# Kernel optimization log

Measured on AMD Instinct MI355X. Metric: run time of the kernel, lower is better.

Reference implementation:

```python
import jax, jax.numpy as jnp
import numpy as np

WS, OWS, NHEAD = 4, 6, 6          # window, overlap window = 4 + int(0.5*4), heads
B, CIN, COU, H, W = 2, 192, 192, 224, 224
MID = CIN  # r = 1


def calc_rpi_oca(ws=WS, ows=OWS):
    # relative position index between ws x ws query window and ows x ows overlapping kv window
    co = np.stack(np.meshgrid(np.arange(ws), np.arange(ws), indexing='ij')).reshape(2, -1)
    ce = np.stack(np.meshgrid(np.arange(ows), np.arange(ows), indexing='ij')).reshape(2, -1)
    rel = (ce[:, None, :] - co[:, :, None]).transpose(1, 2, 0) + (ws - 1)  # [ws*ws, ows*ows, 2], >= 0
    idx = rel[..., 0] * (ws + ows - 1) + rel[..., 1]                       # in [0, (ws+ows-1)^2)
    return jnp.asarray(idx)  # [16, 36]

RPI = calc_rpi_oca()


def conv2d(x, w, b, pad):
    out = jax.lax.conv_general_dilated(x, w, (1, 1), [(pad, pad), (pad, pad)],
                                       dimension_numbers=('NCHW', 'OIHW', 'NCHW'))
    return out + b[None, :, None, None]


def group_norm(x, g, b, groups, eps=1e-5):
    n = x.shape[0]
    xg = x.reshape(n, groups, -1)
    mu = xg.mean(-1, keepdims=True)
    var = xg.var(-1, keepdims=True)
    xn = ((xg - mu) * jax.lax.rsqrt(var + eps)).reshape(x.shape)
    return xn * g[None, :, None, None] + b[None, :, None, None]


def layer_norm(x, g, b, eps=1e-5):
    mu = x.mean(-1, keepdims=True)
    var = x.var(-1, keepdims=True)
    return (x - mu) * jax.lax.rsqrt(var + eps) * g + b


def ocab(x, h, w, ln1_g, ln1_b, qkv_w, qkv_b, rpb, proj_w, proj_b,
         ln2_g, ln2_b, fc1_w, fc1_b, fc2_w, fc2_b):
    b, _, c = x.shape
    nh, nw, d = h // WS, w // WS, c // NHEAD
    shortcut = x
    xn = layer_norm(x, ln1_g, ln1_b).reshape(b, h, w, c)
    qkv = xn @ qkv_w + qkv_b                                  # [b,h,w,3c] laid out [q|k|v]
    q = qkv[..., :c]
    kv = jnp.stack([qkv[..., c:2 * c], qkv[..., 2 * c:]])     # [2,b,h,w,c]
    # non-overlapping query windows -> [b*nwin, 16, NHEAD, d]
    qw = q.reshape(b, nh, WS, nw, WS, c).transpose(0, 1, 3, 2, 4, 5).reshape(b * nh * nw, WS * WS, NHEAD, d)
    # overlapping kv windows = Unfold(kernel=OWS, stride=WS, pad=(OWS-WS)//2)
    pad = (OWS - WS) // 2
    kvp = jnp.pad(kv, ((0, 0), (0, 0), (pad, pad), (pad, pad), (0, 0)))
    rows = (jnp.arange(nh) * WS)[:, None] + jnp.arange(OWS)[None, :]   # [nh, OWS]
    cols = (jnp.arange(nw) * WS)[:, None] + jnp.arange(OWS)[None, :]   # [nw, OWS]
    patches = kvp[:, :, rows[:, None, :, None], cols[None, :, None, :], :]  # [2,b,nh,nw,OWS,OWS,c]
    kvw = patches.reshape(2, b * nh * nw, OWS * OWS, NHEAD, d)
    kw, vw = kvw[0], kvw[1]
    attn = jnp.einsum('wqhd,wkhd->whqk', qw * (d ** -0.5), kw)  # [b*nwin, NHEAD, 16, 36]
    bias = rpb[RPI.reshape(-1)].reshape(WS * WS, OWS * OWS, NHEAD).transpose(2, 0, 1)
    attn = jax.nn.softmax(attn + bias[None], axis=-1)
    out = jnp.einsum('whqk,wkhd->wqhd', attn, vw).reshape(b, nh, nw, WS, WS, c)
    out = out.transpose(0, 1, 3, 2, 4, 5).reshape(b, h * w, c)  # window_reverse
    out = out @ proj_w + proj_b + shortcut
    xm = layer_norm(out, ln2_g, ln2_b)
    mlp = jax.nn.gelu(xm @ fc1_w + fc1_b, approximate=False) @ fc2_w + fc2_b
    return out + mlp


def atoca_forward(x, conv1_w, conv1_b, gn1_g, gn1_b, conv2_w, conv2_b, gn2_g, gn2_b,
                  conv3_w, conv3_b, ln1_g, ln1_b, qkv_w, qkv_b, rpb, proj_w, proj_b,
                  ln2_g, ln2_b, fc1_w, fc1_b, fc2_w, fc2_b):
    Bx, C, Hx, Wx = x.shape
    shortcut = x
    # raw row-major reshape, exactly as the torch code (not a spatial window partition)
    out = x.reshape(Bx * (Hx // WS) * (Wx // WS), C, WS, WS)
    out = conv2d(out, conv1_w, conv1_b, 1)
    out = jax.nn.silu(group_norm(out, gn1_g, gn1_b, NHEAD))
    out = out.transpose(0, 2, 3, 1).reshape(Bx, Hx * Wx, -1)
    out = ocab(out, Hx, Wx, ln1_g, ln1_b, qkv_w, qkv_b, rpb, proj_w, proj_b,
               ln2_g, ln2_b, fc1_w, fc1_b, fc2_w, fc2_b)
    out = out.reshape(Bx * (Hx // WS) * (Wx // WS), WS, WS, -1).transpose(0, 3, 1, 2)
    out = conv2d(out, conv2_w, conv2_b, 1)
    out = group_norm(out, gn2_g, gn2_b, NHEAD)
    out = out.reshape(Bx, -1, Hx, Wx)
    out = out + conv2d(shortcut, conv3_w, conv3_b, 0)
    return jax.nn.relu(out)


def setup_inputs() -> dict:
    key = jax.random.key(0)
    ks = iter(jax.random.split(key, 32))
    rn = lambda shape, s=0.02: (s * jax.random.normal(next(ks), shape)).astype(jnp.float32)
    return {
        'x': jax.random.normal(next(ks), (B, CIN, H, W), dtype=jnp.float32),
        'conv1_w': rn((MID, CIN, 3, 3)), 'conv1_b': rn((MID,)),
        'gn1_g': jnp.ones((MID,), jnp.float32), 'gn1_b': jnp.zeros((MID,), jnp.float32),
        'conv2_w': rn((COU, MID, 3, 3)), 'conv2_b': rn((COU,)),
        'gn2_g': jnp.ones((COU,), jnp.float32), 'gn2_b': jnp.zeros((COU,), jnp.float32),
        'conv3_w': rn((COU, CIN, 1, 1)), 'conv3_b': rn((COU,)),
        'ln1_g': jnp.ones((MID,), jnp.float32), 'ln1_b': jnp.zeros((MID,), jnp.float32),
        'qkv_w': rn((MID, 3 * MID)), 'qkv_b': rn((3 * MID,)),
        'rpb': rn(((WS + OWS - 1) ** 2, NHEAD)),
        'proj_w': rn((MID, MID)), 'proj_b': rn((MID,)),
        'ln2_g': jnp.ones((MID,), jnp.float32), 'ln2_b': jnp.zeros((MID,), jnp.float32),
        'fc1_w': rn((MID, 2 * MID)), 'fc1_b': rn((2 * MID,)),
        'fc2_w': rn((2 * MID, MID)), 'fc2_b': rn((MID,)),
    }


def reference(x, conv1_w, conv1_b, gn1_g, gn1_b, conv2_w, conv2_b, gn2_g, gn2_b,
              conv3_w, conv3_b, ln1_g, ln1_b, qkv_w, qkv_b, rpb, proj_w, proj_b,
              ln2_g, ln2_b, fc1_w, fc1_b, fc2_w, fc2_b):
    return atoca_forward(x, conv1_w, conv1_b, gn1_g, gn1_b, conv2_w, conv2_b, gn2_g, gn2_b,
                         conv3_w, conv3_b, ln1_g, ln1_b, qkv_w, qkv_b, rpb, proj_w, proj_b,
                         ln2_g, ln2_b, fc1_w, fc1_b, fc2_w, fc2_b)
```

## Files before the change

kernel.cpp:

```cpp
#include <hip/hip_runtime.h>
#include <hip/hip_bf16.h>
#include <math.h>

typedef __hip_bfloat16 bf16;
typedef __attribute__((ext_vector_type(8))) short s8v;
typedef __attribute__((ext_vector_type(4))) short s4v;
typedef __attribute__((ext_vector_type(4))) float f32x4;
typedef __attribute__((ext_vector_type(2))) _Float16 h2;

constexpr int CB   = 2;
constexpr int CH   = 224, CW = 224;
constexpr int NHW  = 56;
constexpr int NPATCH = CB * NHW * NHW;
constexpr int TOKPB  = CH * CW;
constexpr int MTOK   = CB * TOKPB;
constexpr size_t SECSZ = 19267584;

constexpr size_t B_T0  = 0;
constexpr size_t B_P2  = B_T0 + 38535168;
constexpr size_t B_P3  = B_P2 + 115605504;
constexpr size_t B_P4  = B_P3 + 38535168;
constexpr size_t B_WF1 = B_P4 + 38535168;
constexpr size_t B_WF2 = B_WF1 + 1327104;
constexpr size_t B_W3F = B_WF2 + 1327104;
constexpr size_t B_WQ  = B_W3F + 147456;
constexpr size_t B_WP  = B_WQ + 221184;
constexpr size_t B_WG1 = B_WP + 73728;
constexpr size_t B_WG2 = B_WG1 + 147456;
constexpr size_t WS_NEEDED = B_WG2 + 147456;

__device__ __forceinline__ float ldf(const float* p) { return *p; }
__device__ __forceinline__ float ldf(const bf16* p)  { return __bfloat162float(*p); }
__device__ __forceinline__ void  stf(float* p, float v) { *p = v; }
__device__ __forceinline__ void  stf(bf16* p, float v)  { *p = __float2bfloat16(v); }
__device__ __forceinline__ unsigned short f2bf(float f) {
    unsigned u = __builtin_bit_cast(unsigned, f);
    unsigned r = (u + 0x7fffu + ((u >> 16) & 1u)) >> 16;
    return (unsigned short)r;
}
__device__ __forceinline__ float bf2f(short s) {
    unsigned u = ((unsigned)(unsigned short)s) << 16;
    return __builtin_bit_cast(float, u);
}

__device__ __forceinline__ void prep_wf(const float* __restrict__ w, short* __restrict__ wf, int o) {
    int within = o & 511, frag = o >> 9;
    int l = within >> 3, j = within & 7;
    int nt = frag % 12, t2 = frag / 12, ks = t2 % 6, tap = t2 / 6;
    int co = nt * 16 + (l & 15);
    int ci = ks * 32 + (l >> 4) * 8 + j;
    wf[o] = (short)f2bf(w[(co * 192 + ci) * 9 + tap]);
}
__device__ __forceinline__ void prep_wgemm(const float* __restrict__ w, short* __restrict__ wf,
                                           int K, int N, int o) {
    int j = o & 7, l = (o >> 3) & 63, f = o >> 9;
    int ntiles = N >> 4;
    int kt = f / ntiles, nt = f % ntiles;
    int k = kt * 32 + (l >> 4) * 8 + j;
    int col = nt * 16 + (l & 15);
    wf[o] = (short)f2bf(w[(size_t)k * N + col]);
}
__device__ __forceinline__ void prep_w3f(const float* __restrict__ w, short* __restrict__ wf, int o) {
    int j = o & 7, l = (o >> 3) & 63, f = o >> 9;
    int kt = f / 12, ct = f % 12;
    int co = ct * 16 + (l & 15);
    int ci = kt * 32 + (l >> 4) * 8 + j;
    wf[o] = (short)f2bf(w[co * 192 + ci]);
}
__global__ __launch_bounds__(256) void prep_all_kernel(
    const float* __restrict__ conv1_w, short* __restrict__ WF1,
    const float* __restrict__ conv2_w, short* __restrict__ WF2,
    const float* __restrict__ conv3_w, short* __restrict__ W3F,
    const float* __restrict__ qkv_w,   short* __restrict__ WQ,
    const float* __restrict__ proj_w,  short* __restrict__ WP,
    const float* __restrict__ fc1_w,   short* __restrict__ WG1,
    const float* __restrict__ fc2_w,   short* __restrict__ WG2)
{
    int o = blockIdx.x * 256 + threadIdx.x;
    if (o < 331776)            { prep_wf(conv1_w, WF1, o); return; }
    o -= 331776;
    if (o < 331776)            { prep_wf(conv2_w, WF2, o); return; }
    o -= 331776;
    if (o < 36864)             { prep_w3f(conv3_w, W3F, o); return; }
    o -= 36864;
    if (o < 110592)            { prep_wgemm(qkv_w, WQ, 192, 576, o); return; }
    o -= 110592;
    if (o < 36864)             { prep_wgemm(proj_w, WP, 192, 192, o); return; }
    o -= 36864;
    if (o < 73728)             { prep_wgemm(fc1_w, WG1, 192, 384, o); return; }
    o -= 73728;
    if (o < 73728)             { prep_wgemm(fc2_w, WG2, 384, 192, o); return; }
}
constexpr int PREP_TOTAL = 331776 * 2 + 36864 + 110592 + 36864 + 73728 * 2;

template <bool FIRST>
__global__ __launch_bounds__(256, 4) void conv_mfma_kernel(
    const void* __restrict__ srcv, const short* __restrict__ wf,
    const float* __restrict__ bias, const float* __restrict__ gng,
    const float* __restrict__ gnb, bf16* __restrict__ dst)
{
    __shared__ short xs[13056];
    __shared__ float gsum[4][6], gsum2[4][6], gmu[4][6], grs[4][6];
    const int tid  = threadIdx.x;
    const int lane = tid & 63, wid = tid >> 6;
    const int n0   = blockIdx.x * 4;

    if (tid < 24) { gsum[tid / 6][tid % 6] = 0.f; gsum2[tid / 6][tid % 6] = 0.f; }
    for (int u = tid; u < 4 * 192; u += 256) {
        int q = u / 192;
        xs[q * 3264 + 3072 + (u % 192)] = 0;
    }

    if constexpr (FIRST) {
        const float4* sp = (const float4*)((const float*)srcv + (size_t)n0 * 3072);
        #pragma unroll
        for (int u = 0; u < 12; ++u) {
            int idx = u * 256 + tid;
            float4 v = sp[idx];
            int q = idx / 768;
            int li = (idx % 768) * 4;
            int ci = li >> 4, p0 = li & 15;
            float vv[4] = { v.x, v.y, v.z, v.w };
            #pragma unroll
            for (int k = 0; k < 4; ++k) {
                int row = p0 + k;
                int ba = q * 6528 + ((row * 384 + ci * 2) ^ ((row & 7) << 4));
                *(short*)((char*)xs + ba) = (short)f2bf(vv[k]);
            }
        }
    } else {
        const s8v* sp8 = (const s8v*)((const bf16*)srcv + (size_t)n0 * 3072);
        #pragma unroll
        for (int u = 0; u < 6; ++u) {
            int li = u * 256 + tid;
            int r = li / 24, ch = li % 24;
            int q = r >> 4, rl = r & 15;
            s8v val = sp8[li];
            int ba = q * 6528 + ((rl * 384 + ch * 16) ^ ((rl & 7) << 4));
            *(s8v*)((char*)xs + ba) = val;
        }
    }
    __syncthreads();

    const int ntb = wid * 3;
    const int cl  = lane & 15;
    const int kg  = lane >> 4;
    f32x4 acc[3][4];
    #pragma unroll
    for (int t = 0; t < 3; ++t) {
        float bv = bias[(ntb + t) * 16 + cl];
        #pragma unroll
        for (int q = 0; q < 4; ++q) acc[t][q] = (f32x4){ bv, bv, bv, bv };
    }

    const int pi = cl >> 2, pj = cl & 3;
    const s8v* wf8 = (const s8v*)wf;

    for (int tap = 0; tap < 9; ++tap) {
        const int di = tap / 3, dj = tap % 3;
        const int ii = pi + di - 1, jj = pj + dj - 1;
        const bool valid = (ii >= 0 && ii < 4 && jj >= 0 && jj < 4);
        const int nr  = valid ? (ii * 4 + jj) : 16;
        const int rb  = nr * 384;
        const int swz = (nr & 7) << 4;
        #pragma unroll
        for (int ks = 0; ks < 6; ++ks) {
            const s8v* bp = wf8 + (size_t)((tap * 6 + ks) * 12) * 64 + lane;
            s8v b0 = bp[(ntb + 0) * 64];
            s8v b1 = bp[(ntb + 1) * 64];
            s8v b2 = bp[(ntb + 2) * 64];
            const int inner = (rb + ks * 64 + kg * 16) ^ swz;
            #pragma unroll
            for (int q = 0; q < 4; ++q) {
                s8v a = *(const s8v*)((const char*)xs + q * 6528 + inner);
                acc[0][q] = __builtin_amdgcn_mfma_f32_16x16x32_bf16(a, b0, acc[0][q], 0, 0, 0);
                acc[1][q] = __builtin_amdgcn_mfma_f32_16x16x32_bf16(a, b1, acc[1][q], 0, 0, 0);
                acc[2][q] = __builtin_amdgcn_mfma_f32_16x16x32_bf16(a, b2, acc[2][q], 0, 0, 0);
            }
        }
    }

    #pragma unroll
    for (int t = 0; t < 3; ++t) {
        const int g = (ntb + t) >> 1;
        #pragma unroll
        for (int q = 0; q < 4; ++q) {
            f32x4 A = acc[t][q];
            float s  = A[0] + A[1] + A[2] + A[3];
            float s2 = A[0]*A[0] + A[1]*A[1] + A[2]*A[2] + A[3]*A[3];
            #pragma unroll
            for (int off = 32; off; off >>= 1) { s += __shfl_xor(s, off); s2 += __shfl_xor(s2, off); }
            if (lane == 0) { atomicAdd(&gsum[q][g], s); atomicAdd(&gsum2[q][g], s2); }
        }
    }
    __syncthreads();
    if (tid < 24) {
        int q = tid / 6, g = tid % 6;
        float mu  = gsum[q][g] * (1.f / 512.f);
        float var = gsum2[q][g] * (1.f / 512.f) - mu * mu;
        gmu[q][g] = mu; grs[q][g] = rsqrtf(var + 1e-5f);
    }
    __syncthreads();

    if constexpr (FIRST) {
        #pragma unroll
        for (int t = 0; t < 3; ++t) {
            const int co = (ntb + t) * 16 + cl, g = (ntb + t) >> 1;
            const float gg = gng[co], gb = gnb[co];
            #pragma unroll
            for (int q = 0; q < 4; ++q) {
                const float mu = gmu[q][g], rs = grs[q][g];
                #pragma unroll
                for (int r = 0; r < 4; ++r) {
                    float v = (acc[t][q][r] - mu) * rs * gg + gb;
                    v = v / (1.f + __expf(-v));
                    int row = q * 16 + kg * 4 + r;
                    int ba = (row * 384 + co * 2) ^ ((row & 7) << 4);
                    *(short*)((char*)xs + ba) = (short)f2bf(v);
                }
            }
        }
        __syncthreads();
        bf16* dp = dst + (size_t)n0 * 3072;
        #pragma unroll
        for (int u = 0; u < 6; ++u) {
            int li = u * 256 + tid;
            int row = li / 24, g2 = li % 24;
            int ba = (row * 384 + g2 * 16) ^ ((row & 7) << 4);
            s8v val = *(const s8v*)((const char*)xs + ba);
            *(s8v*)(dp + (size_t)row * 192 + g2 * 8) = val;
        }
    } else {
        #pragma unroll
        for (int t = 0; t < 3; ++t) {
            const int co = (ntb + t) * 16 + cl, g = (ntb + t) >> 1;
            const float gg = gng[co], gb = gnb[co];
            #pragma unroll
            for (int q = 0; q < 4; ++q) {
                const float mu = gmu[q][g], rs = grs[q][g];
                #pragma unroll
                for (int r = 0; r < 4; ++r) {
                    float v = (acc[t][q][r] - mu) * rs * gg + gb;
                    xs[q * 3072 + co * 16 + kg * 4 + r] = (short)f2bf(v);
                }
            }
        }
        __syncthreads();
        s4v* dp = (s4v*)(dst + (size_t)n0 * 3072);
        const s4v* sps = (const s4v*)xs;
        #pragma unroll
        for (int u = 0; u < 12; ++u) {
            dp[u * 256 + tid] = sps[u * 256 + tid];
        }
    }
}

template <bool RES, bool GELU_ACT, bool LN, bool QKVOUT, int NKT>
__global__ __launch_bounds__(256) void gemm_mfma_kernel(
    const bf16* __restrict__ A, const short* __restrict__ wfb,
    const float* __restrict__ bias, const bf16* __restrict__ res,
    void* __restrict__ out, int N,
    const float* __restrict__ lng, const float* __restrict__ lnb)
{
    __shared__ short ls[8192];
    const int tid = threadIdx.x, lane = tid & 63, wid = tid >> 6;
    const int m0 = blockIdx.x * 128;
    const int cl = lane & 15, kg = lane >> 4;
    constexpr int K = NKT * 32;
    const int ntiles = N >> 4;
    const int ntsec = ntiles / gridDim.y;
    const int ntbeg = blockIdx.y * ntsec;

    s8v af0[NKT], af1[NKT];
    const int r0 = m0 + wid * 32 + cl;
    #pragma unroll
    for (int kt = 0; kt < NKT; ++kt) {
        af0[kt] = *(const s8v*)(A + (size_t)r0 * K + kt * 32 + kg * 8);
        af1[kt] = *(const s8v*)(A + (size_t)(r0 + 16) * K + kt * 32 + kg * 8);
    }
    if constexpr (LN) {
        static_assert(!LN || NKT == 6, "LN requires K==192");
        #pragma unroll
        for (int r = 0; r < 2; ++r) {
            s8v* af = r ? af1 : af0;
            float s = 0.f, s2 = 0.f;
            #pragma unroll
            for (int kt = 0; kt < NKT; ++kt)
                #pragma unroll
                for (int j = 0; j < 8; ++j) {
                    float v = bf2f(af[kt][j]);
                    s += v; s2 += v * v;
                }
            s  += __shfl_xor(s, 16);  s2 += __shfl_xor(s2, 16);
            s  += __shfl_xor(s, 32);  s2 += __shfl_xor(s2, 32);
            const float mu = s * (1.f / 192.f);
            const float rs = rsqrtf(s2 * (1.f / 192.f) - mu * mu + 1e-5f);
            #pragma unroll
            for (int kt = 0; kt < NKT; ++kt) {
                const float* gp = lng + kt * 32 + kg * 8;
                const float* bp = lnb + kt * 32 + kg * 8;
                #pragma unroll
                for (int j = 0; j < 8; ++j) {
                    float v = (bf2f(af[kt][j]) - mu) * rs * gp[j] + bp[j];
                    af[kt][j] = (short)f2bf(v);
                }
            }
        }
    }

    const s8v* wf8 = (const s8v*)wfb;
    for (int nt0 = ntbeg; nt0 < ntbeg + ntsec; nt0 += 4) {
        const int n0 = nt0 * 16;
        f32x4 acc[2][4];
        #pragma unroll
        for (int nf = 0; nf < 4; ++nf) {
            float bv = bias[n0 + nf * 16 + cl];
            acc[0][nf] = (f32x4){ bv, bv, bv, bv };
            acc[1][nf] = (f32x4){ bv, bv, bv, bv };
        }
        #pragma unroll
        for (int kt = 0; kt < NKT; ++kt) {
            #pragma unroll
            for (int nf = 0; nf < 4; ++nf) {
                s8v b = wf8[(size_t)(kt * ntiles + nt0 + nf) * 64 + lane];
                acc[0][nf] = __builtin_amdgcn_mfma_f32_16x16x32_bf16(af0[kt], b, acc[0][nf], 0, 0, 0);
                acc[1][nf] = __builtin_amdgcn_mfma_f32_16x16x32_bf16(af1[kt], b, acc[1][nf], 0, 0, 0);
            }
        }

        __syncthreads();
        #pragma unroll
        for (int rf = 0; rf < 2; ++rf) {
            #pragma unroll
            for (int nf = 0; nf < 4; ++nf) {
                const int lcol = nf * 16 + cl;
                #pragma unroll
                for (int r = 0; r < 4; ++r) {
                    const int lrow = wid * 32 + rf * 16 + kg * 4 + r;
                    float v = acc[rf][nf][r];
                    if (GELU_ACT) v = 0.5f * v * (1.f + erff(v * 0.70710678118f));
                    short sv;
                    if constexpr (QKVOUT) sv = __builtin_bit_cast(short, (_Float16)v);
                    else                  sv = (short)f2bf(v);
                    int ba = (lrow * 128 + lcol * 2) ^ ((lrow & 7) << 4);
                    *(short*)((char*)ls + ba) = sv;
                }
            }
        }
        __syncthreads();
        #pragma unroll
        for (int p = 0; p < 4; ++p) {
            const int lrow = p * 32 + (tid >> 3);
            const int g = tid & 7;
            int ba = (lrow * 128 + g * 16) ^ ((lrow & 7) << 4);
            s8v val = *(const s8v*)((const char*)ls + ba);
            const int row = m0 + lrow;
            const int col0 = n0 + g * 8;
            if constexpr (QKVOUT) {
                const int sec = n0 / 192;
                const int c0 = col0 - sec * 192, h = c0 >> 5, d0 = c0 & 31;
                const int bb2 = row / TOKPB, t = row - bb2 * TOKPB;
                *(s8v*)((_Float16*)out + (size_t)sec * SECSZ +
                        ((size_t)(bb2 * 6 + h) * TOKPB + t) * 32 + d0) = val;
            } else if constexpr (RES) {
                s8v rv = *(const s8v*)(res + (size_t)row * N + col0);
                s8v ov;
                #pragma unroll
                for (int e = 0; e < 8; ++e) ov[e] = (short)f2bf(bf2f(val[e]) + bf2f(rv[e]));
                *(s8v*)((bf16*)out + (size_t)row * N + col0) = ov;
            } else {
                *(s8v*)((bf16*)out + (size_t)row * N + col0) = val;
            }
        }
    }
}

constexpr int HSTR = 1160;
__global__ __launch_bounds__(128) void attn_kernel(
    const _Float16* __restrict__ qf, const float* __restrict__ rpb,
    bf16* __restrict__ out)
{
    __shared__ short kh[6 * HSTR];
    __shared__ short vh[6 * HSTR];
    const int w = blockIdx.x;
    const int b = w / (NHW * NHW), wi = w % (NHW * NHW);
    const int nhi = wi / NHW, nwi = wi % NHW;
    const int tid = threadIdx.x;
    const int r0 = nhi * 4 - 1, c0 = nwi * 4 - 1;
    const _Float16* kfb = qf + SECSZ;
    const _Float16* vfb = qf + 2 * SECSZ;

    #pragma unroll
    for (int it = 0; it < 14; ++it) {
        int v = tid + it * 128;
        if (v < 1728) {
            int kv = v >= 864 ? 1 : 0;
            int u = v - kv * 864;
            int h = u / 144, rem = u % 144, kj = rem >> 2, d0 = (rem & 3) * 8;
            int rr = r0 + kj / 6, cc = c0 + kj % 6;
            s8v val = { 0, 0, 0, 0, 0, 0, 0, 0 };
            if (rr >= 0 && rr < CH && cc >= 0 && cc < CW) {
                const _Float16* src = kv ? vfb : kfb;
                val = *(const s8v*)(src + ((size_t)(b * 6 + h) * TOKPB + rr * CW + cc) * 32 + d0);
            }
            short* dst = kv ? vh : kh;
            *(s8v*)(dst + h * HSTR + kj * 32 + d0) = val;
        }
    }
    __syncthreads();

    if (tid < 96) {
        const int h = tid >> 4, qi = tid & 15;
        const int qr = nhi * 4 + (qi >> 2), qc = nwi * 4 + (qi & 3);
        const _Float16* qp = qf + ((size_t)(b * 6 + h) * TOKPB + qr * CW + qc) * 32;
        h2 qh[16];
        #pragma unroll
        for (int u = 0; u < 4; ++u) {
            uint4 qa = *(const uint4*)(qp + u * 8);
            qh[u * 4 + 0] = __builtin_bit_cast(h2, qa.x);
            qh[u * 4 + 1] = __builtin_bit_cast(h2, qa.y);
            qh[u * 4 + 2] = __builtin_bit_cast(h2, qa.z);
            qh[u * 4 + 3] = __builtin_bit_cast(h2, qa.w);
        }

        float sc[36];
        const short* khb = kh + h * HSTR;
        #pragma unroll
        for (int kj = 0; kj < 36; ++kj) {
            const uint4* kp = (const uint4*)(khb + kj * 32);
            uint4 k0 = kp[0], k1 = kp[1], k2 = kp[2], k3 = kp[3];
            unsigned kwv[16] = { k0.x, k0.y, k0.z, k0.w, k1.x, k1.y, k1.z, k1.w,
                                 k2.x, k2.y, k2.z, k2.w, k3.x, k3.y, k3.z, k3.w };
            float a0 = 0.f, a1 = 0.f, a2 = 0.f, a3 = 0.f;
            #pragma unroll
            for (int e = 0; e < 4; ++e) {
                a0 = __builtin_amdgcn_fdot2(__builtin_bit_cast(h2, kwv[4*e+0]), qh[4*e+0], a0, false);
                a1 = __builtin_amdgcn_fdot2(__builtin_bit_cast(h2, kwv[4*e+1]), qh[4*e+1], a1, false);
                a2 = __builtin_amdgcn_fdot2(__builtin_bit_cast(h2, kwv[4*e+2]), qh[4*e+2], a2, false);
                a3 = __builtin_amdgcn_fdot2(__builtin_bit_cast(h2, kwv[4*e+3]), qh[4*e+3], a3, false);
            }
            const int rel0 = kj / 6 - (qi >> 2) + 3;
            const int rel1 = kj % 6 - (qi & 3) + 3;
            sc[kj] = ((a0 + a1) + (a2 + a3)) * 0.17677669529f + rpb[(rel0 * 9 + rel1) * 6 + h];
        }
        float mx = -1e30f;
        #pragma unroll
        for (int kj = 0; kj < 36; ++kj) mx = fmaxf(mx, sc[kj]);
        float sum = 0.f;
        #pragma unroll
        for (int kj = 0; kj < 36; ++kj) { sc[kj] = __expf(sc[kj] - mx); sum += sc[kj]; }
        const float inv = 1.f / sum;

        h2 o2[16];
        #pragma unroll
        for (int e = 0; e < 16; ++e) o2[e] = (h2){ (_Float16)0.f, (_Float16)0.f };
        const short* vhb = vh + h * HSTR;
        #pragma unroll
        for (int kj = 0; kj < 36; ++kj) {
            const uint4* vp = (const uint4*)(vhb + kj * 32);
            uint4 v0 = vp[0], v1 = vp[1], v2 = vp[2], v3 = vp[3];
            unsigned vwv[16] = { v0.x, v0.y, v0.z, v0.w, v1.x, v1.y, v1.z, v1.w,
                                 v2.x, v2.y, v2.z, v2.w, v3.x, v3.y, v3.z, v3.w };
            const _Float16 ph = (_Float16)sc[kj];
            const h2 ph2 = { ph, ph };
            #pragma unroll
            for (int e = 0; e < 16; ++e)
                o2[e] = __builtin_bit_cast(h2, vwv[e]) * ph2 + o2[e];
        }
        bf16* op = out + ((size_t)(b * TOKPB + qr * CW + qc)) * 192 + h * 32;
        #pragma unroll
        for (int u = 0; u < 8; ++u) {
            s4v pk;
            #pragma unroll
            for (int e = 0; e < 2; ++e) {
                h2 ov = o2[u * 2 + e];
                pk[2 * e]     = (short)f2bf((float)ov[0] * inv);
                pk[2 * e + 1] = (short)f2bf((float)ov[1] * inv);
            }
            *(s4v*)((bf16*)op + u * 4) = pk;
        }
    }
}

__global__ __launch_bounds__(256, 4) void final_mfma_kernel(
    const float* __restrict__ x, const short* __restrict__ w3f,
    const float* __restrict__ b3, const bf16* __restrict__ c2,
    float* __restrict__ out)
{
    __shared__ short xs2[12288];
    const int pix0 = blockIdx.x * 64;
    const int b    = blockIdx.y;
    const int tid = threadIdx.x, lane = tid & 63, wid = tid >> 6;
    const int cl = lane & 15, kg = lane >> 4;
    const float* xb = x + (size_t)b * (192 * TOKPB);

    #pragma unroll
    for (int u = 0; u < 12; ++u) {
        int idx = u * 256 + tid;
        int ci = idx >> 4, p4 = (idx & 15) << 2;
        float4 v = *(const float4*)(xb + (size_t)ci * TOKPB + pix0 + p4);
        float vv[4] = { v.x, v.y, v.z, v.w };
        #pragma unroll
        for (int k = 0; k < 4; ++k) {
            int row = p4 + k;
            int ba = (row * 384 + ci * 2) ^ ((row & 7) << 4);
            *(short*)((char*)xs2 + ba) = (short)f2bf(vv[k]);
        }
    }
    __syncthreads();

    const int ctb = wid * 3;
    f32x4 acc[3][4] = {};
    const s8v* wf8 = (const s8v*)w3f;

    #pragma unroll
    for (int kt = 0; kt < 6; ++kt) {
        s8v a0 = wf8[(size_t)(kt * 12 + ctb + 0) * 64 + lane];
        s8v a1 = wf8[(size_t)(kt * 12 + ctb + 1) * 64 + lane];
        s8v a2 = wf8[(size_t)(kt * 12 + ctb + 2) * 64 + lane];
        #pragma unroll
        for (int pt = 0; pt < 4; ++pt) {
            int row = pt * 16 + cl;
            int ba = (row * 384 + kt * 64 + kg * 16) ^ ((row & 7) << 4);
            s8v bfr = *(const s8v*)((const char*)xs2 + ba);
            acc[0][pt] = __builtin_amdgcn_mfma_f32_16x16x32_bf16(a0, bfr, acc[0][pt], 0, 0, 0);
            acc[1][pt] = __builtin_amdgcn_mfma_f32_16x16x32_bf16(a1, bfr, acc[1][pt], 0, 0, 0);
            acc[2][pt] = __builtin_amdgcn_mfma_f32_16x16x32_bf16(a2, bfr, acc[2][pt], 0, 0, 0);
        }
    }

    #pragma unroll
    for (int t = 0; t < 3; ++t) {
        #pragma unroll
        for (int r = 0; r < 4; ++r) {
            const int co = (ctb + t) * 16 + kg * 4 + r;
            const float bb = b3[co];
            const size_t rowbase = (size_t)b * (192 * TOKPB) + (size_t)co * TOKPB + pix0;
            #pragma unroll
            for (int pt = 0; pt < 4; ++pt) {
                const size_t f = rowbase + pt * 16 + cl;
                float v = acc[t][pt][r] + bb + bf2f(__builtin_bit_cast(short, c2[f]));
                out[f] = fmaxf(v, 0.f);
            }
        }
    }
}

extern "C" void kernel_launch(void* const* d_in, const int* in_sizes, int n_in,
                              void* d_out, int out_size, void* d_ws, size_t ws_size,
                              hipStream_t stream)
{
    if (ws_size < WS_NEEDED) return;

    const float* x       = (const float*)d_in[0];
    const float* conv1_w = (const float*)d_in[1];
    const float* conv1_b = (const float*)d_in[2];
    const float* gn1_g   = (const float*)d_in[3];
    const float* gn1_b   = (const float*)d_in[4];
    const float* conv2_w = (const float*)d_in[5];
    const float* conv2_b = (const float*)d_in[6];
    const float* gn2_g   = (const float*)d_in[7];
    const float* gn2_b   = (const float*)d_in[8];
    const float* conv3_w = (const float*)d_in[9];
    const float* conv3_b = (const float*)d_in[10];
    const float* ln1_g   = (const float*)d_in[11];
    const float* ln1_b   = (const float*)d_in[12];
    const float* qkv_w   = (const float*)d_in[13];
    const float* qkv_b   = (const float*)d_in[14];
    const float* rpb     = (const float*)d_in[15];
    const float* proj_w  = (const float*)d_in[16];
    const float* proj_b  = (const float*)d_in[17];
    const float* ln2_g   = (const float*)d_in[18];
    const float* ln2_b   = (const float*)d_in[19];
    const float* fc1_w   = (const float*)d_in[20];
    const float* fc1_b   = (const float*)d_in[21];
    const float* fc2_w   = (const float*)d_in[22];
    const float* fc2_b   = (const float*)d_in[23];

    char* wsb = (char*)d_ws;
    bf16*  T0  = (bf16*)(wsb + B_T0);
    _Float16* QF = (_Float16*)(wsb + B_P2);
    bf16*  HID = (bf16*)(wsb + B_P2);
    bf16*  P3  = (bf16*)(wsb + B_P3);
    bf16*  P4  = (bf16*)(wsb + B_P4);
    short* WF1 = (short*)(wsb + B_WF1);
    short* WF2 = (short*)(wsb + B_WF2);
    short* W3F = (short*)(wsb + B_W3F);
    short* WQ  = (short*)(wsb + B_WQ);
    short* WP  = (short*)(wsb + B_WP);
    short* WG1 = (short*)(wsb + B_WG1);
    short* WG2 = (short*)(wsb + B_WG2);
    float* OUT = (float*)d_out;

    prep_all_kernel<<<(PREP_TOTAL + 255) / 256, 256, 0, stream>>>(
        conv1_w, WF1, conv2_w, WF2, conv3_w, W3F, qkv_w, WQ, proj_w, WP, fc1_w, WG1, fc2_w, WG2);

    conv_mfma_kernel<true><<<NPATCH / 4, 256, 0, stream>>>(x, WF1, conv1_b, gn1_g, gn1_b, T0);
    gemm_mfma_kernel<false, false, true, true, 6><<<dim3(MTOK / 128, 1), 256, 0, stream>>>(
        T0, WQ, qkv_b, nullptr, QF, 576, ln1_g, ln1_b);
    attn_kernel<<<NPATCH, 128, 0, stream>>>(QF, rpb, P3);
    gemm_mfma_kernel<true, false, false, false, 6><<<dim3(MTOK / 128, 1), 256, 0, stream>>>(
        P3, WP, proj_b, T0, P4, 192, nullptr, nullptr);
    gemm_mfma_kernel<false, true, true, false, 6><<<dim3(MTOK / 128, 1), 256, 0, stream>>>(
        P4, WG1, fc1_b, nullptr, HID, 384, ln2_g, ln2_b);
    gemm_mfma_kernel<true, false, false, false, 12><<<dim3(MTOK / 128, 1), 256, 0, stream>>>(
        HID, WG2, fc2_b, P4, P3, 192, nullptr, nullptr);
    conv_mfma_kernel<false><<<NPATCH / 4, 256, 0, stream>>>(P3, WF2, conv2_b, gn2_g, gn2_b, P4);
    final_mfma_kernel<<<dim3(TOKPB / 64, CB), 256, 0, stream>>>(x, W3F, conv3_b, P4, OUT);
}
```

Baseline: 576.2 us.

## Fuse attention output projection and residual add into attention kernel

The attention kernel now stages its per-window 16x192 output in shared memory and runs the proj GEMM there with MFMA, adding the bias and the T0 residual before writing P4. This removes the separate proj GEMM launch and the round trip of the attention output through global memory. In exchange each 128-thread block reloads the full proj weight fragments from global or L2, only two waves share the MFMA work, and the extra syncthreads and LDS reuse add latency to an already small block.

```diff
diff --git a/kernel.cpp b/kernel.cpp
--- a/kernel.cpp
+++ b/kernel.cpp
@@ -376,16 +376,18 @@
 }
 
 constexpr int HSTR = 1160;
-__global__ __launch_bounds__(128) void attn_kernel(
+__global__ __launch_bounds__(128) void attn_proj_kernel(
     const _Float16* __restrict__ qf, const float* __restrict__ rpb,
-    bf16* __restrict__ out)
+    const short* __restrict__ wpf, const float* __restrict__ pb,
+    const bf16* __restrict__ t0, bf16* __restrict__ omid)
 {
-    __shared__ short kh[6 * HSTR];
-    __shared__ short vh[6 * HSTR];
+    __shared__ __align__(16) short kh[6 * HSTR];
+    __shared__ __align__(16) short vh[6 * HSTR];
     const int w = blockIdx.x;
     const int b = w / (NHW * NHW), wi = w % (NHW * NHW);
     const int nhi = wi / NHW, nwi = wi % NHW;
     const int tid = threadIdx.x;
+    const int lane = tid & 63, wid = tid >> 6;
     const int r0 = nhi * 4 - 1, c0 = nwi * 4 - 1;
     const _Float16* kfb = qf + SECSZ;
     const _Float16* vfb = qf + 2 * SECSZ;
@@ -409,6 +411,8 @@
     }
     __syncthreads();
 
+    h2 o2[16];
+    float inv = 0.f;
     if (tid < 96) {
         const int h = tid >> 4, qi = tid & 15;
         const int qr = nhi * 4 + (qi >> 2), qc = nwi * 4 + (qi & 3);
@@ -449,9 +453,8 @@
         float sum = 0.f;
         #pragma unroll
         for (int kj = 0; kj < 36; ++kj) { sc[kj] = __expf(sc[kj] - mx); sum += sc[kj]; }
-        const float inv = 1.f / sum;
-
-        h2 o2[16];
+        inv = 1.f / sum;
+
         #pragma unroll
         for (int e = 0; e < 16; ++e) o2[e] = (h2){ (_Float16)0.f, (_Float16)0.f };
         const short* vhb = vh + h * HSTR;
@@ -467,18 +470,70 @@
             for (int e = 0; e < 16; ++e)
                 o2[e] = __builtin_bit_cast(h2, vwv[e]) * ph2 + o2[e];
         }
-        bf16* op = out + ((size_t)(b * TOKPB + qr * CW + qc)) * 192 + h * 32;
-        #pragma unroll
-        for (int u = 0; u < 8; ++u) {
-            s4v pk;
-            #pragma unroll
-            for (int e = 0; e < 2; ++e) {
-                h2 ov = o2[u * 2 + e];
+    }
+    __syncthreads();
+
+    if (tid < 96) {
+        const int h = tid >> 4, qi = tid & 15;
+        #pragma unroll
+        for (int u = 0; u < 4; ++u) {
+            s8v pk;
+            #pragma unroll
+            for (int e = 0; e < 4; ++e) {
+                h2 ov = o2[u * 4 + e];
                 pk[2 * e]     = (short)f2bf((float)ov[0] * inv);
                 pk[2 * e + 1] = (short)f2bf((float)ov[1] * inv);
             }
-            *(s4v*)((bf16*)op + u * 4) = pk;
-        }
+            int ba = (qi * 384 + (h * 32 + u * 8) * 2) ^ ((qi & 7) << 4);
+            *(s8v*)((char*)kh + ba) = pk;
+        }
+    }
+    __syncthreads();
+
+    const int cl = lane & 15, kg = lane >> 4;
+    s8v a[6];
+    #pragma unroll
+    for (int kt = 0; kt < 6; ++kt) {
+        int ba = (cl * 384 + kt * 64 + kg * 16) ^ ((cl & 7) << 4);
+        a[kt] = *(const s8v*)((const char*)kh + ba);
+    }
+    f32x4 acc[6];
+    const s8v* wp8 = (const s8v*)wpf;
+    #pragma unroll
+    for (int ctl = 0; ctl < 6; ++ctl) {
+        float bv = pb[(wid * 6 + ctl) * 16 + cl];
+        acc[ctl] = (f32x4){ bv, bv, bv, bv };
+    }
+    #pragma unroll
+    for (int kt = 0; kt < 6; ++kt) {
+        #pragma unroll
+        for (int ctl = 0; ctl < 6; ++ctl) {
+            s8v bfr = wp8[(size_t)(kt * 12 + wid * 6 + ctl) * 64 + lane];
+            acc[ctl] = __builtin_amdgcn_mfma_f32_16x16x32_bf16(a[kt], bfr, acc[ctl], 0, 0, 0);
+        }
+    }
+    #pragma unroll
+    for (int ctl = 0; ctl < 6; ++ctl) {
+        const int col = (wid * 6 + ctl) * 16 + cl;
+        #pragma unroll
+        for (int r = 0; r < 4; ++r) {
+            vh[(kg * 4 + r) * 192 + col] = (short)f2bf(acc[ctl][r]);
+        }
+    }
+    __syncthreads();
+
+    #pragma unroll
+    for (int u = 0; u < 3; ++u) {
+        int li = u * 128 + tid;
+        int row = li / 24, c8 = (li % 24) * 8;
+        int qr = nhi * 4 + (row >> 2), qc = nwi * 4 + (row & 3);
+        size_t gb = ((size_t)(b * TOKPB + qr * CW + qc)) * 192 + c8;
+        s8v pv = *(const s8v*)(vh + row * 192 + c8);
+        s8v rv = *(const s8v*)(t0 + gb);
+        s8v ov;
+        #pragma unroll
+        for (int e = 0; e < 8; ++e) ov[e] = (short)f2bf(bf2f(pv[e]) + bf2f(rv[e]));
+        *(s8v*)(omid + gb) = ov;
     }
 }
 
@@ -598,9 +653,7 @@
     conv_mfma_kernel<true><<<NPATCH / 4, 256, 0, stream>>>(x, WF1, conv1_b, gn1_g, gn1_b, T0);
     gemm_mfma_kernel<false, false, true, true, 6><<<dim3(MTOK / 128, 1), 256, 0, stream>>>(
         T0, WQ, qkv_b, nullptr, QF, 576, ln1_g, ln1_b);
-    attn_kernel<<<NPATCH, 128, 0, stream>>>(QF, rpb, P3);
-    gemm_mfma_kernel<true, false, false, false, 6><<<dim3(MTOK / 128, 1), 256, 0, stream>>>(
-        P3, WP, proj_b, T0, P4, 192, nullptr, nullptr);
+    attn_proj_kernel<<<NPATCH, 128, 0, stream>>>(QF, rpb, WP, proj_b, T0, P4);
     gemm_mfma_kernel<false, true, true, false, 6><<<dim3(MTOK / 128, 1), 256, 0, stream>>>(
         P4, WG1, fc1_b, nullptr, HID, 384, ln2_g, ln2_b);
     gemm_mfma_kernel<true, false, false, false, 12><<<dim3(MTOK / 128, 1), 256, 0, stream>>>(
```

New measurement: 525.6 us. -8.8%, faster.
